# Optimization experiments

Measured on AMD Instinct MI355X. Metric: run time of the kernel, lower is better.

## Reference

```python
import jax, jax.numpy as jnp
import numpy as np


def _local_conv2d(x, w, b):
    """Untied (locally connected) conv, stride 1, VALID.
    x: (B, C, H, W); w: (1, O, C, Ho, Wo, k*k); b: (1, O, Ho, Wo) or None.
    Matches torch: x.unfold(2,k).unfold(3,k) -> (B,C,Ho,Wo,k,k) flattened (k*k),
    then (x[:,None] * w).sum([2,-1]) + b.
    """
    B, C, H, W = x.shape
    Ho, Wo = w.shape[3], w.shape[4]
    kh = H - Ho + 1
    kw = W - Wo + 1
    # patches: (B, C*kh*kw, Ho, Wo), feature dim ordered (C, kh, kw) — same as torch unfold
    patches = jax.lax.conv_general_dilated_patches(x, (kh, kw), (1, 1), 'VALID')
    patches = patches.reshape(B, C, kh * kw, Ho, Wo)
    out = jnp.einsum('bckhw,ochwk->bohw', patches, w[0])
    if b is not None:
        out = out + b
    return out


def _maxpool2(x):
    return jax.lax.reduce_window(x, -jnp.inf, jax.lax.max,
                                 (1, 1, 2, 2), (1, 1, 2, 2), 'VALID')


def setup_inputs() -> dict:
    key = jax.random.key(0)
    ks = jax.random.split(key, 11)
    B, C, H, W = 1024, 3, 32, 32
    s = lambda k, shape, fan: jax.random.normal(k, shape, jnp.float32) * np.sqrt(2.0 / fan)
    return {
        'x': jax.random.normal(ks[0], (B, C, H, W), jnp.float32),
        'w1': s(ks[1], (1, 6, 3, 28, 28, 25), 3 * 25),
        'b1': s(ks[2], (1, 6, 28, 28), 28 * 28) ,
        'w2': s(ks[3], (1, 16, 6, 10, 10, 25), 6 * 25),
        'b2': s(ks[4], (1, 16, 10, 10), 10 * 10),
        'w3': s(ks[5], (1, 120, 16, 1, 1, 25), 16 * 25),
        'b3': s(ks[6], (1, 120, 1, 1), 1),
        'fc2_w': s(ks[7], (84, 120), 120),
        'fc2_b': jnp.zeros((84,), jnp.float32),
        'fc3_w': s(ks[8], (10, 84), 84),
        'fc3_b': jnp.zeros((10,), jnp.float32),
    }


def reference(x, w1, b1, w2, b2, w3, b3, fc2_w, fc2_b, fc3_w, fc3_b):
    h = _maxpool2(jax.nn.relu(_local_conv2d(x, w1, b1)))   # (B,6,14,14)
    h = _maxpool2(jax.nn.relu(_local_conv2d(h, w2, b2)))   # (B,16,5,5)
    h = jax.nn.relu(_local_conv2d(h, w3, b3))              # (B,120,1,1)
    h = h.reshape(h.shape[0], -1)                          # (B,120)
    h = jax.nn.relu(h @ fc2_w.T + fc2_b)                   # (B,84)
    return h @ fc3_w.T + fc3_b                             # (B,10)
```

## Files before the change

### kernel.cpp

```cpp
#include <hip/hip_runtime.h>
#include <math.h>

#define NB 1024

__global__ __launch_bounds__(256) void k_transpose(const float* __restrict__ x,
                                                   float* __restrict__ xT) {
  __shared__ float tile[64][65];
  const int c0 = blockIdx.x * 64;
  const int b0 = blockIdx.y * 64;
  const int tx = threadIdx.x & 63;
  const int ty = threadIdx.x >> 6;
#pragma unroll
  for (int r = 0; r < 16; ++r) {
    const int bb = r * 4 + ty;
    tile[bb][tx] = x[(size_t)(b0 + bb) * 3072 + c0 + tx];
  }
  __syncthreads();
#pragma unroll
  for (int r = 0; r < 16; ++r) {
    const int cc = r * 4 + ty;
    xT[(size_t)(c0 + cc) * NB + b0 + tx] = tile[tx][cc];
  }
}

__global__ __launch_bounds__(256) void k_conv1(const float* __restrict__ xT,
                                               const float* __restrict__ w1,
                                               const float* __restrict__ b1,
                                               float* __restrict__ h1) {
  const int pos = blockIdx.x;
  const int ph = pos / 14, pw = pos % 14;
  const int b = blockIdx.y * 256 + threadIdx.x;

  __shared__ __align__(16) float wL[72 * 28];
  __shared__ float bL[24];
  for (int t = threadIdx.x; t < 72 * 25; t += 256) {
    const int chunk = t / 25, p = t - chunk * 25;
    const int o = chunk / 12, rem = chunk - o * 12;
    const int c = rem >> 2, i = (rem >> 1) & 1, j = rem & 1;
    wL[chunk * 28 + p] =
        w1[((size_t)((o * 3 + c) * 28 + (2 * ph + i)) * 28 + (2 * pw + j)) * 25 + p];
  }
  if (threadIdx.x < 24) {
    const int o = threadIdx.x >> 2, i = (threadIdx.x >> 1) & 1, j = threadIdx.x & 1;
    bL[threadIdx.x] = b1[(size_t)(o * 28 + (2 * ph + i)) * 28 + (2 * pw + j)];
  }
  __syncthreads();

  float acc[6][2][2];
#pragma unroll
  for (int o = 0; o < 6; ++o)
#pragma unroll
    for (int i = 0; i < 2; ++i)
#pragma unroll
      for (int j = 0; j < 2; ++j) acc[o][i][j] = 0.f;

  for (int c = 0; c < 3; ++c) {
    float xw[6][6];
#pragma unroll
    for (int dh = 0; dh < 6; ++dh)
#pragma unroll
      for (int dw = 0; dw < 6; ++dw)
        xw[dh][dw] =
            xT[((size_t)(c * 32 + (2 * ph + dh)) * 32 + (2 * pw + dw)) * NB + b];
#pragma unroll
    for (int o = 0; o < 6; ++o)
#pragma unroll
      for (int i = 0; i < 2; ++i)
#pragma unroll
        for (int j = 0; j < 2; ++j) {
          const float* wp = &wL[((o * 3 + c) * 4 + i * 2 + j) * 28];
#pragma unroll
          for (int p = 0; p < 25; ++p)
            acc[o][i][j] = fmaf(xw[i + p / 5][j + p % 5], wp[p], acc[o][i][j]);
        }
  }

#pragma unroll
  for (int o = 0; o < 6; ++o) {
    float v[2][2];
#pragma unroll
    for (int i = 0; i < 2; ++i)
#pragma unroll
      for (int j = 0; j < 2; ++j)
        v[i][j] = fmaxf(acc[o][i][j] + bL[o * 4 + i * 2 + j], 0.f);
    const float m = fmaxf(fmaxf(v[0][0], v[0][1]), fmaxf(v[1][0], v[1][1]));
    h1[((size_t)(o * 14 + ph) * 14 + pw) * NB + b] = m;
  }
}

__global__ __launch_bounds__(256) void k_conv2(const float* __restrict__ h1,
                                               const float* __restrict__ w2,
                                               const float* __restrict__ b2,
                                               float* __restrict__ h2) {
  const int pos = blockIdx.x;
  const int ph = pos / 5, pw = pos - 5 * (pos / 5);
  const int og = blockIdx.y;
  const int b = blockIdx.z * 256 + threadIdx.x;

  __shared__ __align__(16) float wL[96 * 28];
  __shared__ float bL[16];
  for (int t = threadIdx.x; t < 96 * 25; t += 256) {
    const int chunk = t / 25, p = t - chunk * 25;
    const int oo = chunk / 24, rem = chunk - oo * 24;
    const int c = rem >> 2, i = (rem >> 1) & 1, j = rem & 1;
    const int o = og * 4 + oo;
    wL[chunk * 28 + p] =
        w2[((size_t)((o * 6 + c) * 10 + (2 * ph + i)) * 10 + (2 * pw + j)) * 25 + p];
  }
  if (threadIdx.x < 16) {
    const int oo = threadIdx.x >> 2, i = (threadIdx.x >> 1) & 1, j = threadIdx.x & 1;
    const int o = og * 4 + oo;
    bL[threadIdx.x] = b2[(size_t)(o * 10 + (2 * ph + i)) * 10 + (2 * pw + j)];
  }
  __syncthreads();

  float acc[4][2][2];
#pragma unroll
  for (int oo = 0; oo < 4; ++oo)
#pragma unroll
    for (int i = 0; i < 2; ++i)
#pragma unroll
      for (int j = 0; j < 2; ++j) acc[oo][i][j] = 0.f;

  for (int c = 0; c < 6; ++c) {
    float xw[6][6];
#pragma unroll
    for (int dh = 0; dh < 6; ++dh)
#pragma unroll
      for (int dw = 0; dw < 6; ++dw)
        xw[dh][dw] =
            h1[((size_t)(c * 14 + (2 * ph + dh)) * 14 + (2 * pw + dw)) * NB + b];
#pragma unroll
    for (int oo = 0; oo < 4; ++oo)
#pragma unroll
      for (int i = 0; i < 2; ++i)
#pragma unroll
        for (int j = 0; j < 2; ++j) {
          const float* wp = &wL[((oo * 6 + c) * 4 + i * 2 + j) * 28];
#pragma unroll
          for (int p = 0; p < 25; ++p)
            acc[oo][i][j] = fmaf(xw[i + p / 5][j + p % 5], wp[p], acc[oo][i][j]);
        }
  }

#pragma unroll
  for (int oo = 0; oo < 4; ++oo) {
    const int o = og * 4 + oo;
    float v[2][2];
#pragma unroll
    for (int i = 0; i < 2; ++i)
#pragma unroll
      for (int j = 0; j < 2; ++j)
        v[i][j] = fmaxf(acc[oo][i][j] + bL[oo * 4 + i * 2 + j], 0.f);
    const float m = fmaxf(fmaxf(v[0][0], v[0][1]), fmaxf(v[1][0], v[1][1]));
    h2[((size_t)(o * 5 + ph) * 5 + pw) * NB + b] = m;
  }
}

__global__ __launch_bounds__(256) void k_conv3(const float* __restrict__ h2,
                                               const float* __restrict__ w3,
                                               const float* __restrict__ b3,
                                               float* __restrict__ h3) {
  const int o = blockIdx.x;
  const int b = blockIdx.y * 256 + threadIdx.x;
  __shared__ __align__(16) float wL[400];
  for (int t = threadIdx.x; t < 400; t += 256) wL[t] = w3[(size_t)o * 400 + t];
  __syncthreads();

  float a0 = 0.f, a1 = 0.f, a2 = 0.f, a3 = 0.f;
#pragma unroll 8
  for (int k = 0; k < 400; k += 4) {
    a0 = fmaf(h2[(size_t)(k + 0) * NB + b], wL[k + 0], a0);
    a1 = fmaf(h2[(size_t)(k + 1) * NB + b], wL[k + 1], a1);
    a2 = fmaf(h2[(size_t)(k + 2) * NB + b], wL[k + 2], a2);
    a3 = fmaf(h2[(size_t)(k + 3) * NB + b], wL[k + 3], a3);
  }
  h3[(size_t)o * NB + b] = fmaxf((a0 + a1) + (a2 + a3) + b3[o], 0.f);
}

__global__ __launch_bounds__(256) void k_fc2(const float* __restrict__ h3,
                                             const float* __restrict__ fc2w,
                                             const float* __restrict__ fc2b,
                                             float* __restrict__ h4) {
  const int b = blockIdx.x * 64 + (threadIdx.x & 63);
  const int jj = threadIdx.x >> 6;
  const int j = blockIdx.y * 4 + jj;
  __shared__ __align__(16) float wL[4 * 120];
  for (int t = threadIdx.x; t < 480; t += 256)
    wL[t] = fc2w[(size_t)blockIdx.y * 480 + t];
  __syncthreads();

  const float* __restrict__ wp = &wL[jj * 120];
  float a0 = 0.f, a1 = 0.f;
#pragma unroll
  for (int k = 0; k < 120; k += 2) {
    a0 = fmaf(h3[(size_t)(k + 0) * NB + b], wp[k + 0], a0);
    a1 = fmaf(h3[(size_t)(k + 1) * NB + b], wp[k + 1], a1);
  }
  h4[(size_t)j * NB + b] = fmaxf(a0 + a1 + fc2b[j], 0.f);
}

__global__ __launch_bounds__(256) void k_fc3(const float* __restrict__ h4,
                                             const float* __restrict__ fc3w,
                                             const float* __restrict__ fc3b,
                                             float* __restrict__ out) {
  const int b = blockIdx.x * 64 + (threadIdx.x & 63);
  const int ii = threadIdx.x >> 6;
  const int i = blockIdx.y * 4 + ii;
  __shared__ __align__(16) float wL[4 * 84];
  for (int t = threadIdx.x; t < 336; t += 256) {
    const int gi = blockIdx.y * 336 + t;
    wL[t] = (gi < 840) ? fc3w[gi] : 0.f;
  }
  __syncthreads();

  if (i < 10) {
    const float* __restrict__ wp = &wL[ii * 84];
    float a0 = 0.f, a1 = 0.f;
#pragma unroll
    for (int j = 0; j < 84; j += 2) {
      a0 = fmaf(h4[(size_t)(j + 0) * NB + b], wp[j + 0], a0);
      a1 = fmaf(h4[(size_t)(j + 1) * NB + b], wp[j + 1], a1);
    }
    out[(size_t)b * 10 + i] = a0 + a1 + fc3b[i];
  }
}

extern "C" void kernel_launch(void* const* d_in, const int* in_sizes, int n_in,
                              void* d_out, int out_size, void* d_ws, size_t ws_size,
                              hipStream_t stream) {
  const float* x    = (const float*)d_in[0];
  const float* w1   = (const float*)d_in[1];
  const float* b1   = (const float*)d_in[2];
  const float* w2   = (const float*)d_in[3];
  const float* b2   = (const float*)d_in[4];
  const float* w3   = (const float*)d_in[5];
  const float* b3   = (const float*)d_in[6];
  const float* fc2w = (const float*)d_in[7];
  const float* fc2b = (const float*)d_in[8];
  const float* fc3w = (const float*)d_in[9];
  const float* fc3b = (const float*)d_in[10];
  float* out = (float*)d_out;

  float* ws = (float*)d_ws;
  float* xT = ws;
  float* h1 = xT + 3145728;
  float* h2 = h1 + 1204224;
  float* h3 = h2 + 409600;
  float* h4 = xT;

  k_transpose<<<dim3(48, 16), 256, 0, stream>>>(x, xT);
  k_conv1<<<dim3(196, 4), 256, 0, stream>>>(xT, w1, b1, h1);
  k_conv2<<<dim3(25, 4, 4), 256, 0, stream>>>(h1, w2, b2, h2);
  k_conv3<<<dim3(120, 4), 256, 0, stream>>>(h2, w3, b3, h3);
  k_fc2<<<dim3(16, 21), 256, 0, stream>>>(h3, fc2w, fc2b, h4);
  k_fc3<<<dim3(16, 3), 256, 0, stream>>>(h4, fc3w, fc3b, out);
}
```

Baseline: 171.4 us.

## Swizzle block indices per XCD, split conv2 output groups, fuse FC layers

After: 168.3 us. About the same (-1.8%).

```diff
diff --git a/kernel.cpp b/kernel.cpp
--- a/kernel.cpp
+++ b/kernel.cpp
@@ -27,9 +27,12 @@
                                                const float* __restrict__ w1,
                                                const float* __restrict__ b1,
                                                float* __restrict__ h1) {
-  const int pos = blockIdx.x;
+  const int w = blockIdx.x;
+  const int xcd = w & 7, k = w >> 3;
+  const int bg = xcd >> 1;
+  const int pos = (xcd & 1) * 98 + k;
   const int ph = pos / 14, pw = pos % 14;
-  const int b = blockIdx.y * 256 + threadIdx.x;
+  const int b = bg * 256 + threadIdx.x;
 
   __shared__ __align__(16) float wL[72 * 28];
   __shared__ float bL[24];
@@ -92,31 +95,35 @@
                                                const float* __restrict__ w2,
                                                const float* __restrict__ b2,
                                                float* __restrict__ h2) {
-  const int pos = blockIdx.x;
-  const int ph = pos / 5, pw = pos - 5 * (pos / 5);
-  const int og = blockIdx.y;
-  const int b = blockIdx.z * 256 + threadIdx.x;
-
-  __shared__ __align__(16) float wL[96 * 28];
-  __shared__ float bL[16];
-  for (int t = threadIdx.x; t < 96 * 25; t += 256) {
+  const int w = blockIdx.x;
+  const int xcd = w & 7, k = w >> 3;
+  const int bg = xcd >> 1;
+  const int unit = (xcd & 1) * 100 + k;
+  const int og = unit / 25;
+  const int pos = unit % 25;
+  const int ph = pos / 5, pw = pos % 5;
+  const int b = bg * 256 + threadIdx.x;
+
+  __shared__ __align__(16) float wL[48 * 28];
+  __shared__ float bL[8];
+  for (int t = threadIdx.x; t < 48 * 25; t += 256) {
     const int chunk = t / 25, p = t - chunk * 25;
     const int oo = chunk / 24, rem = chunk - oo * 24;
     const int c = rem >> 2, i = (rem >> 1) & 1, j = rem & 1;
-    const int o = og * 4 + oo;
+    const int o = og * 2 + oo;
     wL[chunk * 28 + p] =
         w2[((size_t)((o * 6 + c) * 10 + (2 * ph + i)) * 10 + (2 * pw + j)) * 25 + p];
   }
-  if (threadIdx.x < 16) {
+  if (threadIdx.x < 8) {
     const int oo = threadIdx.x >> 2, i = (threadIdx.x >> 1) & 1, j = threadIdx.x & 1;
-    const int o = og * 4 + oo;
+    const int o = og * 2 + oo;
     bL[threadIdx.x] = b2[(size_t)(o * 10 + (2 * ph + i)) * 10 + (2 * pw + j)];
   }
   __syncthreads();
 
-  float acc[4][2][2];
-#pragma unroll
-  for (int oo = 0; oo < 4; ++oo)
+  float acc[2][2][2];
+#pragma unroll
+  for (int oo = 0; oo < 2; ++oo)
 #pragma unroll
     for (int i = 0; i < 2; ++i)
 #pragma unroll
@@ -131,7 +138,7 @@
         xw[dh][dw] =
             h1[((size_t)(c * 14 + (2 * ph + dh)) * 14 + (2 * pw + dw)) * NB + b];
 #pragma unroll
-    for (int oo = 0; oo < 4; ++oo)
+    for (int oo = 0; oo < 2; ++oo)
 #pragma unroll
       for (int i = 0; i < 2; ++i)
 #pragma unroll
@@ -144,8 +151,8 @@
   }
 
 #pragma unroll
-  for (int oo = 0; oo < 4; ++oo) {
-    const int o = og * 4 + oo;
+  for (int oo = 0; oo < 2; ++oo) {
+    const int o = og * 2 + oo;
     float v[2][2];
 #pragma unroll
     for (int i = 0; i < 2; ++i)
@@ -161,8 +168,11 @@
                                                const float* __restrict__ w3,
                                                const float* __restrict__ b3,
                                                float* __restrict__ h3) {
-  const int o = blockIdx.x;
-  const int b = blockIdx.y * 256 + threadIdx.x;
+  const int w = blockIdx.x;
+  const int xcd = w & 7, k2 = w >> 3;
+  const int bg = xcd >> 1;
+  const int o = (xcd & 1) * 60 + k2;
+  const int b = bg * 256 + threadIdx.x;
   __shared__ __align__(16) float wL[400];
   for (int t = threadIdx.x; t < 400; t += 256) wL[t] = w3[(size_t)o * 400 + t];
   __syncthreads();
@@ -178,51 +188,53 @@
   h3[(size_t)o * NB + b] = fmaxf((a0 + a1) + (a2 + a3) + b3[o], 0.f);
 }
 
-__global__ __launch_bounds__(256) void k_fc2(const float* __restrict__ h3,
-                                             const float* __restrict__ fc2w,
-                                             const float* __restrict__ fc2b,
-                                             float* __restrict__ h4) {
-  const int b = blockIdx.x * 64 + (threadIdx.x & 63);
-  const int jj = threadIdx.x >> 6;
-  const int j = blockIdx.y * 4 + jj;
-  __shared__ __align__(16) float wL[4 * 120];
-  for (int t = threadIdx.x; t < 480; t += 256)
-    wL[t] = fc2w[(size_t)blockIdx.y * 480 + t];
-  __syncthreads();
-
-  const float* __restrict__ wp = &wL[jj * 120];
-  float a0 = 0.f, a1 = 0.f;
-#pragma unroll
-  for (int k = 0; k < 120; k += 2) {
-    a0 = fmaf(h3[(size_t)(k + 0) * NB + b], wp[k + 0], a0);
-    a1 = fmaf(h3[(size_t)(k + 1) * NB + b], wp[k + 1], a1);
-  }
-  h4[(size_t)j * NB + b] = fmaxf(a0 + a1 + fc2b[j], 0.f);
-}
-
-__global__ __launch_bounds__(256) void k_fc3(const float* __restrict__ h4,
-                                             const float* __restrict__ fc3w,
-                                             const float* __restrict__ fc3b,
-                                             float* __restrict__ out) {
-  const int b = blockIdx.x * 64 + (threadIdx.x & 63);
-  const int ii = threadIdx.x >> 6;
-  const int i = blockIdx.y * 4 + ii;
-  __shared__ __align__(16) float wL[4 * 84];
-  for (int t = threadIdx.x; t < 336; t += 256) {
-    const int gi = blockIdx.y * 336 + t;
-    wL[t] = (gi < 840) ? fc3w[gi] : 0.f;
-  }
-  __syncthreads();
-
-  if (i < 10) {
-    const float* __restrict__ wp = &wL[ii * 84];
+__global__ __launch_bounds__(256) void k_fctail(const float* __restrict__ h3,
+                                                const float* __restrict__ fc2w,
+                                                const float* __restrict__ fc2b,
+                                                const float* __restrict__ fc3w,
+                                                const float* __restrict__ fc3b,
+                                                float* __restrict__ out) {
+  const int b0 = blockIdx.x * 16;
+  const int tid = threadIdx.x;
+  __shared__ float h3L[120 * 16];
+  __shared__ float h4L[84 * 16];
+
+  for (int t = tid; t < 120 * 16; t += 256) {
+    const int k = t >> 4, bb = t & 15;
+    h3L[t] = h3[(size_t)k * NB + b0 + bb];
+  }
+  __syncthreads();
+
+  const int bb = tid & 15;
+  {
+    const int jbase = tid >> 4;
+#pragma unroll
+    for (int jr = 0; jr < 6; ++jr) {
+      const int j = jbase + jr * 16;
+      if (j < 84) {
+        const float* __restrict__ wp = fc2w + (size_t)j * 120;
+        float a0 = 0.f, a1 = 0.f;
+#pragma unroll
+        for (int k = 0; k < 120; k += 2) {
+          a0 = fmaf(h3L[(k + 0) * 16 + bb], wp[k + 0], a0);
+          a1 = fmaf(h3L[(k + 1) * 16 + bb], wp[k + 1], a1);
+        }
+        h4L[j * 16 + bb] = fmaxf(a0 + a1 + fc2b[j], 0.f);
+      }
+    }
+  }
+  __syncthreads();
+
+  if (tid < 160) {
+    const int i = tid >> 4;
+    const float* __restrict__ wp = fc3w + (size_t)i * 84;
     float a0 = 0.f, a1 = 0.f;
 #pragma unroll
     for (int j = 0; j < 84; j += 2) {
-      a0 = fmaf(h4[(size_t)(j + 0) * NB + b], wp[j + 0], a0);
-      a1 = fmaf(h4[(size_t)(j + 1) * NB + b], wp[j + 1], a1);
+      a0 = fmaf(h4L[(j + 0) * 16 + bb], wp[j + 0], a0);
+      a1 = fmaf(h4L[(j + 1) * 16 + bb], wp[j + 1], a1);
     }
-    out[(size_t)b * 10 + i] = a0 + a1 + fc3b[i];
+    out[(size_t)(b0 + bb) * 10 + i] = a0 + a1 + fc3b[i];
   }
 }
 
@@ -247,12 +259,10 @@
   float* h1 = xT + 3145728;
   float* h2 = h1 + 1204224;
   float* h3 = h2 + 409600;
-  float* h4 = xT;
 
   k_transpose<<<dim3(48, 16), 256, 0, stream>>>(x, xT);
-  k_conv1<<<dim3(196, 4), 256, 0, stream>>>(xT, w1, b1, h1);
-  k_conv2<<<dim3(25, 4, 4), 256, 0, stream>>>(h1, w2, b2, h2);
-  k_conv3<<<dim3(120, 4), 256, 0, stream>>>(h2, w3, b3, h3);
-  k_fc2<<<dim3(16, 21), 256, 0, stream>>>(h3, fc2w, fc2b, h4);
-  k_fc3<<<dim3(16, 3), 256, 0, stream>>>(h4, fc3w, fc3b, out);
-}
+  k_conv1<<<dim3(784), 256, 0, stream>>>(xT, w1, b1, h1);
+  k_conv2<<<dim3(800), 256, 0, stream>>>(h1, w2, b2, h2);
+  k_conv3<<<dim3(480), 256, 0, stream>>>(h2, w3, b3, h3);
+  k_fctail<<<dim3(64), 256, 0, stream>>>(h3, fc2w, fc2b, fc3w, fc3b, out);
+}
```
